# Kernel optimization log

Hardware: AMD Instinct MI355X
Metric: run time of the kernel (lower is better)

## Reference

```python
import jax, jax.numpy as jnp
import numpy as np


def setup_inputs() -> dict:
    key = jax.random.key(0)
    k1, k2 = jax.random.split(key)
    B, V, K = 8, 50000, 128
    # eigenvalues of a Laplacian are non-negative; use uniform [0, 1)
    evals = jax.random.uniform(k1, (B, K), dtype=jnp.float32)
    evecs = jax.random.normal(k2, (B, V, K), dtype=jnp.float32)
    return {"evals": evals, "evecs": evecs, "count": 16}


def reference(evals, evecs, count):
    # scales = logspace(-2, 0, count) in base 10 (matches torch.logspace)
    scales = jnp.power(jnp.asarray(10.0, evals.dtype),
                       jnp.linspace(-2.0, 0.0, count, dtype=evals.dtype))  # [count]
    # coefs[b, c, k] = exp(-evals[b, k] * scales[c])
    coefs = jnp.exp(-evals[:, None, :] * scales[None, :, None])  # [B, count, K]
    # out[b, v, c] = sum_k evecs[b, v, k]^2 * coefs[b, c, k]  (batched GEMM,
    # avoids materializing the naive [B, V, count, K] intermediate)
    return jnp.einsum('bvk,bck->bvc', evecs * evecs, coefs)
```

## Files before the change

kernel.cpp:

```cpp
#include <hip/hip_runtime.h>


constexpr int B_  = 8;
constexpr int V_  = 50000;
constexpr int K_  = 128;
constexpr int CNT = 16;
constexpr int TPB = 256;
constexpr int VT  = V_ / 16;
constexpr int TOT = B_ * VT;
constexpr int TPW = 2;
constexpr int NBLK = TOT / (4 * TPW);

typedef short bf16x8 __attribute__((ext_vector_type(8)));
typedef float f32x4  __attribute__((ext_vector_type(4)));

static __device__ __forceinline__ unsigned short f2bf(float f) {
    union { float f; unsigned u; } v; v.f = f;
    unsigned r = v.u + 0x7FFFu + ((v.u >> 16) & 1u);
    return (unsigned short)(r >> 16);
}

__global__ void fill_coef(const float* __restrict__ evals,
                          unsigned short* __restrict__ coefB) {
    const int b = blockIdx.x;
    for (int i = threadIdx.x; i < CNT * K_; i += blockDim.x) {
        const int c = i >> 7;
        const int k = i & (K_ - 1);
        const float s = powf(10.0f, -2.0f + (float)c * (2.0f / 15.0f));
        coefB[b * CNT * K_ + i] = f2bf(expf(-evals[b * K_ + k] * s));
    }
}

__global__ __launch_bounds__(TPB) void heat_mfma(
    const float* __restrict__ evecs,
    const unsigned short* __restrict__ coefB,
    float* __restrict__ out)
{
    const int lane = threadIdx.x & 63;
    const int gw   = blockIdx.x * 4 + (threadIdx.x >> 6);
    const int r    = lane & 15;
    const int kg   = lane >> 4;

    const int t0 = gw * TPW;

    float4 a[TPW][8];
    bf16x8 bf[TPW][4];
    long   vbase[TPW];

#pragma unroll
    for (int t = 0; t < TPW; ++t) {
        const int tile = t0 + t;
        const int b    = tile / VT;
        const int vt   = tile - b * VT;
        vbase[t] = (long)b * V_ + (long)vt * 16;

        const float* arow =
            evecs + (vbase[t] + r) * K_ + kg * 8;
        const unsigned short* brow =
            coefB + ((long)b * CNT + r) * K_ + kg * 8;
#pragma unroll
        for (int m = 0; m < 4; ++m) {
            a[t][2 * m]     = *(const float4*)(arow + m * 32);
            a[t][2 * m + 1] = *(const float4*)(arow + m * 32 + 4);
            bf[t][m]        = *(const bf16x8*)(brow + m * 32);
        }
    }

#pragma unroll
    for (int t = 0; t < TPW; ++t) {
        f32x4 acc = {0.f, 0.f, 0.f, 0.f};
#pragma unroll
        for (int m = 0; m < 4; ++m) {
            const float4 e0 = a[t][2 * m];
            const float4 e1 = a[t][2 * m + 1];
            bf16x8 af;
            af[0] = (short)f2bf(e0.x * e0.x);
            af[1] = (short)f2bf(e0.y * e0.y);
            af[2] = (short)f2bf(e0.z * e0.z);
            af[3] = (short)f2bf(e0.w * e0.w);
            af[4] = (short)f2bf(e1.x * e1.x);
            af[5] = (short)f2bf(e1.y * e1.y);
            af[6] = (short)f2bf(e1.z * e1.z);
            af[7] = (short)f2bf(e1.w * e1.w);
            acc = __builtin_amdgcn_mfma_f32_16x16x32_bf16(af, bf[t][m], acc,
                                                          0, 0, 0);
        }
#pragma unroll
        for (int i = 0; i < 4; ++i)
            out[(vbase[t] + kg * 4 + i) * CNT + r] = acc[i];
    }
}

extern "C" void kernel_launch(void* const* d_in, const int* in_sizes, int n_in,
                              void* d_out, int out_size, void* d_ws, size_t ws_size,
                              hipStream_t stream) {
    const float* evals = (const float*)d_in[0];
    const float* evecs = (const float*)d_in[1];
    float* out = (float*)d_out;
    unsigned short* coefB = (unsigned short*)d_ws;

    fill_coef<<<B_, 256, 0, stream>>>(evals, coefB);
    heat_mfma<<<NBLK, TPB, 0, stream>>>(evecs, coefB, out);
}
```

Baseline: 47.19 us.

## Fuse coefficient computation into MFMA kernel and use 2D grid per batch

Removes the separate fill_coef launch and instead computes the bf16 exp coefficients inside each wave from evals, using exp2f for the scale and the fast __expf. The grid becomes 2D (v-tiles by batch), with bounds-guarded tail tiles, and the output is written with nontemporal stores. The goal is to drop one kernel launch and the workspace round-trip. The cost is redundant exp work in every wave and lower precision from __expf.

```diff
diff --git a/kernel.cpp b/kernel.cpp
--- a/kernel.cpp
+++ b/kernel.cpp
@@ -7,9 +7,9 @@
 constexpr int CNT = 16;
 constexpr int TPB = 256;
 constexpr int VT  = V_ / 16;
-constexpr int TOT = B_ * VT;
 constexpr int TPW = 2;
-constexpr int NBLK = TOT / (4 * TPW);
+constexpr int TPBLK = 4 * TPW;
+constexpr int GX  = (VT + TPBLK - 1) / TPBLK;
 
 typedef short bf16x8 __attribute__((ext_vector_type(8)));
 typedef float f32x4  __attribute__((ext_vector_type(4)));
@@ -20,50 +20,52 @@
     return (unsigned short)(r >> 16);
 }
 
-__global__ void fill_coef(const float* __restrict__ evals,
-                          unsigned short* __restrict__ coefB) {
-    const int b = blockIdx.x;
-    for (int i = threadIdx.x; i < CNT * K_; i += blockDim.x) {
-        const int c = i >> 7;
-        const int k = i & (K_ - 1);
-        const float s = powf(10.0f, -2.0f + (float)c * (2.0f / 15.0f));
-        coefB[b * CNT * K_ + i] = f2bf(expf(-evals[b * K_ + k] * s));
-    }
-}
-
 __global__ __launch_bounds__(TPB) void heat_mfma(
+    const float* __restrict__ evals,
     const float* __restrict__ evecs,
-    const unsigned short* __restrict__ coefB,
     float* __restrict__ out)
 {
     const int lane = threadIdx.x & 63;
-    const int gw   = blockIdx.x * 4 + (threadIdx.x >> 6);
+    const int wid  = threadIdx.x >> 6;
+    const int b    = blockIdx.y;
     const int r    = lane & 15;
     const int kg   = lane >> 4;
 
-    const int t0 = gw * TPW;
+    const int vt0 = (blockIdx.x * 4 + wid) * TPW;
 
     float4 a[TPW][8];
-    bf16x8 bf[TPW][4];
     long   vbase[TPW];
-
+    bool   valid[TPW];
 #pragma unroll
     for (int t = 0; t < TPW; ++t) {
-        const int tile = t0 + t;
-        const int b    = tile / VT;
-        const int vt   = tile - b * VT;
+        int vt   = vt0 + t;
+        valid[t] = (vt < VT);
+        vt       = valid[t] ? vt : (VT - 1);
         vbase[t] = (long)b * V_ + (long)vt * 16;
-
-        const float* arow =
-            evecs + (vbase[t] + r) * K_ + kg * 8;
-        const unsigned short* brow =
-            coefB + ((long)b * CNT + r) * K_ + kg * 8;
+        const float* arow = evecs + (vbase[t] + r) * K_ + kg * 8;
 #pragma unroll
         for (int m = 0; m < 4; ++m) {
             a[t][2 * m]     = *(const float4*)(arow + m * 32);
             a[t][2 * m + 1] = *(const float4*)(arow + m * 32 + 4);
-            bf[t][m]        = *(const bf16x8*)(brow + m * 32);
         }
+    }
+
+    const float s = exp2f(fmaf((float)r, 0.4429237459849816f,
+                               -6.6438561897747246f));
+    const float* evb = evals + b * K_ + kg * 8;
+    bf16x8 bf[4];
+#pragma unroll
+    for (int m = 0; m < 4; ++m) {
+        const float4 e0 = *(const float4*)(evb + m * 32);
+        const float4 e1 = *(const float4*)(evb + m * 32 + 4);
+        bf[m][0] = (short)f2bf(__expf(-e0.x * s));
+        bf[m][1] = (short)f2bf(__expf(-e0.y * s));
+        bf[m][2] = (short)f2bf(__expf(-e0.z * s));
+        bf[m][3] = (short)f2bf(__expf(-e0.w * s));
+        bf[m][4] = (short)f2bf(__expf(-e1.x * s));
+        bf[m][5] = (short)f2bf(__expf(-e1.y * s));
+        bf[m][6] = (short)f2bf(__expf(-e1.z * s));
+        bf[m][7] = (short)f2bf(__expf(-e1.w * s));
     }
 
 #pragma unroll
@@ -82,12 +84,15 @@
             af[5] = (short)f2bf(e1.y * e1.y);
             af[6] = (short)f2bf(e1.z * e1.z);
             af[7] = (short)f2bf(e1.w * e1.w);
-            acc = __builtin_amdgcn_mfma_f32_16x16x32_bf16(af, bf[t][m], acc,
+            acc = __builtin_amdgcn_mfma_f32_16x16x32_bf16(af, bf[m], acc,
                                                           0, 0, 0);
         }
+        if (valid[t]) {
 #pragma unroll
-        for (int i = 0; i < 4; ++i)
-            out[(vbase[t] + kg * 4 + i) * CNT + r] = acc[i];
+            for (int i = 0; i < 4; ++i)
+                __builtin_nontemporal_store(
+                    acc[i], &out[(vbase[t] + kg * 4 + i) * CNT + r]);
+        }
     }
 }
 
@@ -97,8 +102,7 @@
     const float* evals = (const float*)d_in[0];
     const float* evecs = (const float*)d_in[1];
     float* out = (float*)d_out;
-    unsigned short* coefB = (unsigned short*)d_ws;
 
-    fill_coef<<<B_, 256, 0, stream>>>(evals, coefB);
-    heat_mfma<<<NBLK, TPB, 0, stream>>>(evecs, coefB, out);
+    dim3 grid(GX, B_);
+    heat_mfma<<<grid, TPB, 0, stream>>>(evals, evecs, out);
 }
```

After: 39.60 us. 16.1% less time.
